# Kernel tuning notes

Hardware: AMD Instinct MI355X
Metric: run time of the kernel (lower is better)

The kernel has to match this reference:

```python
import jax, jax.numpy as jnp
import numpy as np
from jax import lax

BETA = 0.9   # membrane decay
THR = 1.0    # firing threshold (soft reset)
K = 10       # number of time bins
# spatial pyramid for original_shape=(100,368) under 4 stride-2 SAME convs
HW = [(50, 184), (25, 92), (13, 46), (7, 23)]
CH = [4, 8, 16, 32]


def conv(x, w, b, stride=1):
    y = lax.conv_general_dilated(x, w, (stride, stride), 'SAME',
                                 dimension_numbers=('NCHW', 'OIHW', 'NCHW'))
    return y + b[None, :, None, None]


def spike(u):
    # heaviside forward, sigmoid straight-through surrogate backward
    s = (u > 0.0).astype(u.dtype)
    sg = jax.nn.sigmoid(4.0 * u)
    return sg + lax.stop_gradient(s - sg)


def setup_inputs() -> dict:
    key = jax.random.key(0)
    ks = jax.random.split(key, 12)
    T, B = 1000, 1
    x = jax.random.normal(ks[0], (T, B, 1, 100, 368), jnp.float32)

    def w(k, o, i, kh=3, kw=3):
        return 0.1 * jax.random.normal(k, (o, i, kh, kw), jnp.float32)

    inp = {'x': x}
    cin = [1] + CH[:3]
    for li in range(4):
        inp['w%d' % (li + 1)] = w(ks[1 + li], CH[li], cin[li])
        inp['b%d' % (li + 1)] = jnp.zeros((CH[li],), jnp.float32)
    sc = [2 * K * c for c in CH]  # skip channels: [80,160,320,640]
    inp['dw4'] = w(ks[5], 64, sc[3]); inp['db4'] = jnp.zeros((64,), jnp.float32)
    inp['dw3'] = w(ks[6], 32, 64 + sc[2]); inp['db3'] = jnp.zeros((32,), jnp.float32)
    inp['dw2'] = w(ks[7], 16, 32 + sc[1]); inp['db2'] = jnp.zeros((16,), jnp.float32)
    inp['dw1'] = w(ks[8], 8, 16 + sc[0]); inp['db1'] = jnp.zeros((8,), jnp.float32)
    inp['wo'] = w(ks[9], 1, 8, 1, 1); inp['bo'] = jnp.zeros((1,), jnp.float32)
    inp['total_steps'] = 1000
    inp['block_size'] = 100
    return inp


def reference(x, w1, b1, w2, b2, w3, b3, w4, b4,
              dw4, db4, dw3, db3, dw2, db2, dw1, db1, wo, bo,
              total_steps, block_size):
    S = total_steps // K  # steps per bin
    B = x.shape[1]
    xb = x.reshape((K, S) + x.shape[1:])  # [K,S,B,C,H,W]
    mems0 = tuple(jnp.zeros((B, CH[i], HW[i][0], HW[i][1]), x.dtype) for i in range(4))
    enc_w = [(w1, b1), (w2, b2), (w3, b3), (w4, b4)]

    def forward_step(x_t, mems):
        new_mems, spk = [], x_t
        for (wi, bi), m in zip(enc_w, mems):
            m = BETA * m + conv(spk, wi, bi, 2)
            spk = spike(m - THR)
            m = m - spk * THR  # soft reset
            new_mems.append(m)
        return tuple(new_mems)

    def step(carry, x_t):
        mems, sums, sqs = carry
        mems = forward_step(x_t, mems)
        sums = tuple(s + m for s, m in zip(sums, mems))
        sqs = tuple(q + m * m for q, m in zip(sqs, mems))
        return (mems, sums, sqs), None

    def bin_fn(mems, x_bin):
        zeros = tuple(jnp.zeros_like(m) for m in mems)
        (mems, sums, sqs), _ = lax.scan(step, (mems, zeros, zeros), x_bin)
        means = tuple(s / S for s in sums)
        stds = tuple(jnp.sqrt(jnp.maximum(q / S - mu * mu, 1e-8))
                     for q, mu in zip(sqs, means))
        return mems, (means, stds)

    _, (means, stds) = lax.scan(bin_fn, mems0, xb)  # each leaf: [K,B,C,H,W]

    def skip(mean, std):
        # torch.cat([mean0,std0,mean1,std1,...], dim=1) channel ordering
        f = jnp.stack([mean, std], axis=1)        # [K,2,B,C,H,W]
        f = jnp.transpose(f, (2, 0, 1, 3, 4, 5))  # [B,K,2,C,H,W]
        b_, k_, t_, c_, h_, w_ = f.shape
        return f.reshape(b_, k_ * t_ * c_, h_, w_)

    skips = [skip(means[i], stds[i]) for i in range(4)]

    def up(t, hw):
        return jax.image.resize(t, (t.shape[0], t.shape[1], hw[0], hw[1]), 'bilinear')

    relu = jax.nn.relu
    d = relu(conv(skips[3], dw4, db4))
    d = relu(conv(jnp.concatenate([up(d, HW[2]), skips[2]], 1), dw3, db3))
    d = relu(conv(jnp.concatenate([up(d, HW[1]), skips[1]], 1), dw2, db2))
    d = relu(conv(jnp.concatenate([up(d, HW[0]), skips[0]], 1), dw1, db1))
    tau_c = conv(up(d, (100, 368)), wo, bo)  # [B,1,100,368]
    return tau_c
```

## Files before the change

### kernel.cpp

```cpp
#include <hip/hip_runtime.h>

#define KBINS  10
#define SBIN   100
#define BETA   0.9f
#define THR    1.0f
#define CDIV(a,b) (((a)+(b)-1)/(b))


__global__ void k_zero16(float4* __restrict__ p, int n16) {
    int i = blockIdx.x * blockDim.x + threadIdx.x;
    if (i < n16) p[i] = make_float4(0.f, 0.f, 0.f, 0.f);
}

__global__ void k_conv1(const float* __restrict__ x,
                        const float* __restrict__ w1,
                        const float* __restrict__ b1,
                        float* __restrict__ c1) {
    int n = blockIdx.x * blockDim.x + threadIdx.x;
    if (n >= 1000 * 50 * 46) return;
    int wq  = n % 46;
    int tmp = n / 46;
    int h   = tmp % 50;
    int t   = tmp / 50;
    int w0  = wq * 4;

    const float* xt = x + (size_t)t * 36800;
    float rm2 = (h  < 49)  ? 1.f : 0.f;
    float cm8 = (w0 < 180) ? 1.f : 0.f;
    int   r2  = min(2 * h + 2, 99);
    int   cb  = 2 * w0;
    int   c8  = min(cb + 8, 367);

    const float* row0 = xt + (2 * h) * 368 + cb;
    const float* row1 = row0 + 368;
    const float* row2 = xt + r2 * 368 + cb;

    float tap[3][9];
    #pragma unroll
    for (int j = 0; j < 8; j++) {
        tap[0][j] = row0[j];
        tap[1][j] = row1[j];
        tap[2][j] = row2[j] * rm2;
    }
    tap[0][8] = xt[(2 * h) * 368 + c8] * cm8;
    tap[1][8] = xt[(2 * h + 1) * 368 + c8] * cm8;
    tap[2][8] = xt[r2 * 368 + c8] * (rm2 * cm8);

    float* ot = c1 + (size_t)t * 36800 + h * 184 + w0;
    #pragma unroll
    for (int co = 0; co < 4; co++) {
        float b = b1[co];
        float a0 = b, a1 = b, a2 = b, a3 = b;
        #pragma unroll
        for (int r = 0; r < 3; r++) {
            #pragma unroll
            for (int kw = 0; kw < 3; kw++) {
                float wv = w1[co * 9 + r * 3 + kw];
                a0 = fmaf(tap[r][0 + kw], wv, a0);
                a1 = fmaf(tap[r][2 + kw], wv, a1);
                a2 = fmaf(tap[r][4 + kw], wv, a2);
                a3 = fmaf(tap[r][6 + kw], wv, a3);
            }
        }
        *(float4*)(ot + (size_t)co * 9200) = make_float4(a0, a1, a2, a3);
    }
}

__global__ void k_scan(const float* __restrict__ cbuf,
                       unsigned char* __restrict__ spk,
                       float* __restrict__ skip,
                       int C, int HW, int Win, int Wp, int HpWp, int write_spk) {
    const int PF = 10;
    int CHW = C * HW;
    int p = blockIdx.x * blockDim.x + threadIdx.x;
    if (p >= CHW) return;
    int c  = p / HW;
    int hw = p - c * HW;
    int h  = hw / Win, w = hw - h * Win;

    unsigned char* sp = spk + (size_t)c * HpWp + (h + 1) * Wp + (w + 1);
    const size_t tstr = (size_t)C * HpWp;

    float m = 0.0f;
    float va[PF], vb[PF];
    #pragma unroll
    for (int j = 0; j < PF; j++) va[j] = cbuf[(size_t)j * CHW + p];

    for (int k = 0; k < KBINS; k++) {
        float s = 0.0f, q = 0.0f;
        for (int b = 0; b < SBIN / PF; b++) {
            int t0 = k * SBIN + b * PF;
            int tn = t0 + PF;
            bool more = (tn < KBINS * SBIN);
            #pragma unroll
            for (int j = 0; j < PF; j++)
                vb[j] = more ? cbuf[(size_t)(tn + j) * CHW + p] : 0.0f;
            #pragma unroll
            for (int j = 0; j < PF; j++) {
                m = fmaf(m, BETA, va[j]);
                float spv = (m - THR > 0.0f) ? 1.0f : 0.0f;
                m -= spv * THR;
                if (write_spk) sp[(size_t)(t0 + j) * tstr] = (unsigned char)spv;
                s += m;
                q = fmaf(m, m, q);
            }
            #pragma unroll
            for (int j = 0; j < PF; j++) va[j] = vb[j];
        }
        float mean = s * (1.0f / SBIN);
        float var  = q * (1.0f / SBIN) - mean * mean;
        float sd   = sqrtf(fmaxf(var, 1e-8f));
        skip[(size_t)(k * 2 * C + c) * HW + hw]     = mean;
        skip[(size_t)(k * 2 * C + C + c) * HW + hw] = sd;
    }
}

template<int CIN, int COUT, int COG, int OW,
         int HOUT, int WOUT, int PADH, int HP, int WP>
__global__ void k_convs2(const unsigned char* __restrict__ spk,
                         const float* __restrict__ wt,
                         const float* __restrict__ bias,
                         float* __restrict__ out) {
    const int WQ = (WOUT + OW - 1) / OW;
    const int NT = 2 * OW + 1;
    int n = blockIdx.x * blockDim.x + threadIdx.x;
    if (n >= 1000 * HOUT * WQ) return;
    int wq  = n % WQ;
    int tmp = n / WQ;
    int h   = tmp % HOUT;
    int t   = tmp / HOUT;
    int cog = blockIdx.y;
    int w0  = wq * OW;

    const unsigned char* base = spk + (size_t)t * CIN * HP * WP
                              + (2 * h - PADH + 1) * WP + (2 * w0 + 1);

    float acc[OW][COG];
    #pragma unroll
    for (int q = 0; q < OW; q++)
        #pragma unroll
        for (int co = 0; co < COG; co++) acc[q][co] = bias[cog * COG + co];

    for (int ci = 0; ci < CIN; ci++) {
        const unsigned char* ic = base + (size_t)ci * HP * WP;
        float tap[3][NT];
        #pragma unroll
        for (int r = 0; r < 3; r++)
            #pragma unroll
            for (int j = 0; j < NT; j++)
                tap[r][j] = (float)ic[r * WP + j];
        #pragma unroll
        for (int co = 0; co < COG; co++) {
            const float* wc = wt + ((size_t)(cog * COG + co) * CIN + ci) * 9;
            #pragma unroll
            for (int r = 0; r < 3; r++)
                #pragma unroll
                for (int kw = 0; kw < 3; kw++) {
                    float wv = wc[r * 3 + kw];
                    #pragma unroll
                    for (int q = 0; q < OW; q++)
                        acc[q][co] = fmaf(tap[r][2 * q + kw], wv, acc[q][co]);
                }
        }
    }

    float* ot = out + ((size_t)t * COUT + cog * COG) * (HOUT * WOUT) + h * WOUT + w0;
    #pragma unroll
    for (int co = 0; co < COG; co++) {
        float* oc = ot + (size_t)co * (HOUT * WOUT);
        if constexpr (OW == 4) {
            *(float4*)oc = make_float4(acc[0][co], acc[1][co], acc[2][co], acc[3][co]);
        } else {
            if (w0 + 2 <= WOUT) *(float2*)oc = make_float2(acc[0][co], acc[1][co]);
            else                oc[0] = acc[0][co];
        }
    }
}

__global__ void k_conv_part(const float* __restrict__ in, int Cin, int H, int W,
                            const float* __restrict__ wt,
                            float* __restrict__ part,
                            int Cout, int CS) {
    int HW  = H * W;
    int pix = blockIdx.x * blockDim.x + threadIdx.x;
    if (pix >= HW) return;
    int co    = blockIdx.y;
    int chunk = blockIdx.z;
    int h = pix / W, w = pix - h * W;

    int off[9]; float msk[9];
    #pragma unroll
    for (int kh = 0; kh < 3; kh++) {
        int r = h + kh - 1;
        bool rok = (r >= 0) && (r < H);
        int rc = rok ? r : 0;
        #pragma unroll
        for (int kw = 0; kw < 3; kw++) {
            int cc = w + kw - 1;
            bool cok = (cc >= 0) && (cc < W);
            int ccc = cok ? cc : 0;
            off[kh * 3 + kw] = rc * W + ccc;
            msk[kh * 3 + kw] = (rok && cok) ? 1.0f : 0.0f;
        }
    }

    const float* ibase = in + (size_t)chunk * CS * HW;
    const float* wbase = wt + ((size_t)co * Cin + (size_t)chunk * CS) * 9;
    float acc = 0.0f;
    #pragma unroll 2
    for (int ci = 0; ci < CS; ci++) {
        const float* ic = ibase + (size_t)ci * HW;
        const float* wc = wbase + ci * 9;
        #pragma unroll
        for (int j = 0; j < 9; j++)
            acc = fmaf(msk[j] * ic[off[j]], wc[j], acc);
    }
    part[((size_t)chunk * Cout + co) * HW + pix] = acc;
}

__global__ void k_reduce_relu(const float* __restrict__ part,
                              const float* __restrict__ bias,
                              float* __restrict__ out,
                              int Cout, int HW, int nchunks) {
    int n = blockIdx.x * blockDim.x + threadIdx.x;
    if (n >= Cout * HW) return;
    int co = n / HW;
    float acc = bias[co];
    for (int c = 0; c < nchunks; c++)
        acc += part[(size_t)c * Cout * HW + n];
    out[n] = fmaxf(acc, 0.0f);
}

__global__ void k_up_cat(const float* __restrict__ up_src, int Cup, int Hi, int Wi,
                         const float* __restrict__ skip, int Cskip,
                         float* __restrict__ out, int Ho, int Wo) {
    int total = (Cup + Cskip) * Ho * Wo;
    int n = blockIdx.x * blockDim.x + threadIdx.x;
    if (n >= total) return;
    int w   = n % Wo;
    int tmp = n / Wo;
    int h   = tmp % Ho;
    int c   = tmp / Ho;
    float v;
    if (c < Cup) {
        float ph = (h + 0.5f) * (float)Hi / (float)Ho - 0.5f;
        float pw = (w + 0.5f) * (float)Wi / (float)Wo - 0.5f;
        float fh = floorf(ph), fw = floorf(pw);
        int h0 = (int)fh, w0 = (int)fw;
        float ah = ph - fh, aw = pw - fw;
        int h0c = min(max(h0, 0), Hi - 1), h1c = min(max(h0 + 1, 0), Hi - 1);
        int w0c = min(max(w0, 0), Wi - 1), w1c = min(max(w0 + 1, 0), Wi - 1);
        const float* sc = up_src + (size_t)c * Hi * Wi;
        float v00 = sc[h0c * Wi + w0c], v01 = sc[h0c * Wi + w1c];
        float v10 = sc[h1c * Wi + w0c], v11 = sc[h1c * Wi + w1c];
        v = (1.0f - ah) * ((1.0f - aw) * v00 + aw * v01)
          + ah * ((1.0f - aw) * v10 + aw * v11);
    } else {
        v = skip[(size_t)(c - Cup) * Ho * Wo + h * Wo + w];
    }
    out[n] = v;
}

__global__ void k_final(const float* __restrict__ d1,
                        const float* __restrict__ wo,
                        const float* __restrict__ bo,
                        float* __restrict__ out) {
    int n = blockIdx.x * blockDim.x + threadIdx.x;
    if (n >= 36800) return;
    int w = n % 368, h = n / 368;
    float ph = (h + 0.5f) * 0.5f - 0.5f;
    float pw = (w + 0.5f) * 0.5f - 0.5f;
    float fh = floorf(ph), fw = floorf(pw);
    int h0 = (int)fh, w0 = (int)fw;
    float ah = ph - fh, aw = pw - fw;
    int h0c = min(max(h0, 0), 49),  h1c = min(max(h0 + 1, 0), 49);
    int w0c = min(max(w0, 0), 183), w1c = min(max(w0 + 1, 0), 183);
    float acc = bo[0];
    #pragma unroll
    for (int c = 0; c < 8; c++) {
        const float* sc = d1 + c * 9200;
        float v00 = sc[h0c * 184 + w0c], v01 = sc[h0c * 184 + w1c];
        float v10 = sc[h1c * 184 + w0c], v11 = sc[h1c * 184 + w1c];
        float v = (1.0f - ah) * ((1.0f - aw) * v00 + aw * v01)
                + ah * ((1.0f - aw) * v10 + aw * v11);
        acc = fmaf(wo[c], v, acc);
    }
    out[n] = acc;
}

extern "C" void kernel_launch(void* const* d_in, const int* in_sizes, int n_in,
                              void* d_out, int out_size, void* d_ws, size_t ws_size,
                              hipStream_t stream) {
    (void)in_sizes; (void)n_in; (void)out_size; (void)ws_size;
    const float* x   = (const float*)d_in[0];
    const float* w1  = (const float*)d_in[1];
    const float* b1  = (const float*)d_in[2];
    const float* w2  = (const float*)d_in[3];
    const float* b2  = (const float*)d_in[4];
    const float* w3  = (const float*)d_in[5];
    const float* b3  = (const float*)d_in[6];
    const float* w4  = (const float*)d_in[7];
    const float* b4  = (const float*)d_in[8];
    const float* dw4 = (const float*)d_in[9];
    const float* db4 = (const float*)d_in[10];
    const float* dw3 = (const float*)d_in[11];
    const float* db3 = (const float*)d_in[12];
    const float* dw2 = (const float*)d_in[13];
    const float* db2 = (const float*)d_in[14];
    const float* dw1 = (const float*)d_in[15];
    const float* db1 = (const float*)d_in[16];
    const float* wo  = (const float*)d_in[17];
    const float* bo  = (const float*)d_in[18];
    float* out = (float*)d_out;

    char* ws = (char*)d_ws;
    size_t off = 0;
    auto alloc = [&](size_t bytes) -> void* {
        void* p = ws + off;
        off += (bytes + 255) & ~(size_t)255;
        return p;
    };
    float*         cbuf  = (float*)alloc(147200000);
    unsigned char* spk1p = (unsigned char*)alloc(39936000);
    unsigned char* spk2p = (unsigned char*)alloc(21600000);
    unsigned char* spk3p = (unsigned char*)alloc(12960000);
    float*         skip0 = (float*)alloc(2944000);
    float*         skip1 = (float*)alloc(1472000);
    float*         skip2 = (float*)alloc(765440);
    float*         skip3 = (float*)alloc(412160);
    char* dec = (char*)cbuf;
    size_t doff = 0;
    auto dalloc = [&](size_t bytes) -> void* {
        void* p = dec + doff;
        doff += (bytes + 255) & ~(size_t)255;
        return p;
    };
    float* d4   = (float*)dalloc(10304u * 4);
    float* cat3 = (float*)dalloc(229632u * 4);
    float* d3   = (float*)dalloc(19136u * 4);
    float* cat2 = (float*)dalloc(441600u * 4);
    float* d2   = (float*)dalloc(36800u * 4);
    float* cat1 = (float*)dalloc(883200u * 4);
    float* d1   = (float*)dalloc(73600u * 4);
    float* part = (float*)dalloc(1048576u);

    const int BS  = 256;
    const int SBS = 64;

    {
        int n16 = (39936000 + 21600000 + 12960000) / 16;
        k_zero16<<<CDIV(n16, BS), BS, 0, stream>>>((float4*)spk1p, n16);
    }

    k_conv1<<<CDIV(1000 * 50 * 46, BS), BS, 0, stream>>>(x, w1, b1, cbuf);
    k_scan<<<CDIV(36800, SBS), SBS, 0, stream>>>(cbuf, spk1p, skip0,
                                                 4, 9200, 184, 192, 52 * 192, 1);

    k_convs2<4, 8, 8, 4, 25, 92, 0, 52, 192>
        <<<dim3(CDIV(1000 * 25 * 23, BS), 1), BS, 0, stream>>>(spk1p, w2, b2, cbuf);
    k_scan<<<CDIV(18400, SBS), SBS, 0, stream>>>(cbuf, spk2p, skip1,
                                                 8, 2300, 92, 100, 27 * 100, 1);

    k_convs2<8, 16, 16, 2, 13, 46, 1, 27, 100>
        <<<dim3(CDIV(1000 * 13 * 23, BS), 1), BS, 0, stream>>>(spk2p, w3, b3, cbuf);
    k_scan<<<CDIV(9568, SBS), SBS, 0, stream>>>(cbuf, spk3p, skip2,
                                                16, 598, 46, 54, 15 * 54, 1);

    k_convs2<16, 32, 16, 2, 7, 23, 1, 15, 54>
        <<<dim3(CDIV(1000 * 7 * 12, BS), 2), BS, 0, stream>>>(spk3p, w4, b4, cbuf);
    k_scan<<<CDIV(5152, SBS), SBS, 0, stream>>>(cbuf, spk3p , skip3,
                                                32, 161, 23, 31, 9 * 31, 0);

    {
        dim3 g(CDIV(161, BS), 64, 10);
        k_conv_part<<<g, BS, 0, stream>>>(skip3, 640, 7, 23, dw4, part, 64, 64);
        k_reduce_relu<<<CDIV(64 * 161, BS), BS, 0, stream>>>(part, db4, d4, 64, 161, 10);
    }
    k_up_cat<<<CDIV(384 * 598, BS), BS, 0, stream>>>(d4, 64, 7, 23,
                                                     skip2, 320, cat3, 13, 46);
    {
        dim3 g(CDIV(598, BS), 32, 8);
        k_conv_part<<<g, BS, 0, stream>>>(cat3, 384, 13, 46, dw3, part, 32, 48);
        k_reduce_relu<<<CDIV(32 * 598, BS), BS, 0, stream>>>(part, db3, d3, 32, 598, 8);
    }
    k_up_cat<<<CDIV(192 * 2300, BS), BS, 0, stream>>>(d3, 32, 13, 46,
                                                      skip1, 160, cat2, 25, 92);
    {
        dim3 g(CDIV(2300, BS), 16, 4);
        k_conv_part<<<g, BS, 0, stream>>>(cat2, 192, 25, 92, dw2, part, 16, 48);
        k_reduce_relu<<<CDIV(16 * 2300, BS), BS, 0, stream>>>(part, db2, d2, 16, 2300, 4);
    }
    k_up_cat<<<CDIV(96 * 9200, BS), BS, 0, stream>>>(d2, 16, 25, 92,
                                                     skip0, 80, cat1, 50, 184);
    {
        dim3 g(CDIV(9200, BS), 8, 2);
        k_conv_part<<<g, BS, 0, stream>>>(cat1, 96, 50, 184, dw1, part, 8, 48);
        k_reduce_relu<<<CDIV(8 * 9200, BS), BS, 0, stream>>>(part, db1, d1, 8, 9200, 2);
    }
    k_final<<<CDIV(36800, BS), BS, 0, stream>>>(d1, wo, bo, out);
}
```

Measured before the change: 1.001 ms.

## Chunk encoder over time to shrink the conv buffer and fuse upsample-concat into decoder conv

The layer-1 and layer-2 conv plus scan stages now run in time chunks (5 and 2 chunks), with membrane state carried between chunks, so the fp32 conv buffer shrinks from about 147 MB to about 38 MB and can stay more cache-resident. The separate upsample/concat kernels are removed; a new decoder conv kernel computes the bilinear upsample on the fly and reads skip features directly. The cost is more kernel launches, serial dependencies between chunks, and repeated interpolation work inside the conv. Some decoder block sizes also change and the partial-conv loop uses two accumulators.

```diff
diff --git a/kernel.cpp b/kernel.cpp
--- a/kernel.cpp
+++ b/kernel.cpp
@@ -15,9 +15,9 @@
 __global__ void k_conv1(const float* __restrict__ x,
                         const float* __restrict__ w1,
                         const float* __restrict__ b1,
-                        float* __restrict__ c1) {
+                        float* __restrict__ c1, int tcount) {
     int n = blockIdx.x * blockDim.x + threadIdx.x;
-    if (n >= 1000 * 50 * 46) return;
+    if (n >= tcount * 50 * 46) return;
     int wq  = n % 46;
     int tmp = n / 46;
     int h   = tmp % 50;
@@ -69,7 +69,9 @@
 __global__ void k_scan(const float* __restrict__ cbuf,
                        unsigned char* __restrict__ spk,
                        float* __restrict__ skip,
-                       int C, int HW, int Win, int Wp, int HpWp, int write_spk) {
+                       float* __restrict__ mstate,
+                       int C, int HW, int Win, int Wp, int HpWp,
+                       int write_spk, int bin0, int nbins, int init) {
     const int PF = 10;
     int CHW = C * HW;
     int p = blockIdx.x * blockDim.x + threadIdx.x;
@@ -78,41 +80,45 @@
     int hw = p - c * HW;
     int h  = hw / Win, w = hw - h * Win;
 
-    unsigned char* sp = spk + (size_t)c * HpWp + (h + 1) * Wp + (w + 1);
     const size_t tstr = (size_t)C * HpWp;
-
-    float m = 0.0f;
+    unsigned char* sp = spk + (size_t)bin0 * SBIN * tstr
+                      + (size_t)c * HpWp + (h + 1) * Wp + (w + 1);
+
+    float m = init ? 0.0f : mstate[p];
     float va[PF], vb[PF];
     #pragma unroll
     for (int j = 0; j < PF; j++) va[j] = cbuf[(size_t)j * CHW + p];
 
-    for (int k = 0; k < KBINS; k++) {
+    int T = nbins * SBIN;
+    for (int k = 0; k < nbins; k++) {
         float s = 0.0f, q = 0.0f;
         for (int b = 0; b < SBIN / PF; b++) {
-            int t0 = k * SBIN + b * PF;
-            int tn = t0 + PF;
-            bool more = (tn < KBINS * SBIN);
+            int lt0 = k * SBIN + b * PF;
+            int ltn = lt0 + PF;
+            bool more = (ltn < T);
             #pragma unroll
             for (int j = 0; j < PF; j++)
-                vb[j] = more ? cbuf[(size_t)(tn + j) * CHW + p] : 0.0f;
+                vb[j] = more ? cbuf[(size_t)(ltn + j) * CHW + p] : 0.0f;
             #pragma unroll
             for (int j = 0; j < PF; j++) {
                 m = fmaf(m, BETA, va[j]);
                 float spv = (m - THR > 0.0f) ? 1.0f : 0.0f;
                 m -= spv * THR;
-                if (write_spk) sp[(size_t)(t0 + j) * tstr] = (unsigned char)spv;
+                if (write_spk) sp[(size_t)(lt0 + j) * tstr] = (unsigned char)spv;
                 s += m;
                 q = fmaf(m, m, q);
             }
             #pragma unroll
             for (int j = 0; j < PF; j++) va[j] = vb[j];
         }
+        int g = bin0 + k;
         float mean = s * (1.0f / SBIN);
         float var  = q * (1.0f / SBIN) - mean * mean;
         float sd   = sqrtf(fmaxf(var, 1e-8f));
-        skip[(size_t)(k * 2 * C + c) * HW + hw]     = mean;
-        skip[(size_t)(k * 2 * C + C + c) * HW + hw] = sd;
-    }
+        skip[(size_t)(g * 2 * C + c) * HW + hw]     = mean;
+        skip[(size_t)(g * 2 * C + C + c) * HW + hw] = sd;
+    }
+    mstate[p] = m;
 }
 
 template<int CIN, int COUT, int COG, int OW,
@@ -120,19 +126,19 @@
 __global__ void k_convs2(const unsigned char* __restrict__ spk,
                          const float* __restrict__ wt,
                          const float* __restrict__ bias,
-                         float* __restrict__ out) {
+                         float* __restrict__ out, int t0, int tcount) {
     const int WQ = (WOUT + OW - 1) / OW;
     const int NT = 2 * OW + 1;
     int n = blockIdx.x * blockDim.x + threadIdx.x;
-    if (n >= 1000 * HOUT * WQ) return;
+    if (n >= tcount * HOUT * WQ) return;
     int wq  = n % WQ;
     int tmp = n / WQ;
     int h   = tmp % HOUT;
-    int t   = tmp / HOUT;
+    int tl  = tmp / HOUT;
     int cog = blockIdx.y;
     int w0  = wq * OW;
 
-    const unsigned char* base = spk + (size_t)t * CIN * HP * WP
+    const unsigned char* base = spk + (size_t)(t0 + tl) * CIN * HP * WP
                               + (2 * h - PADH + 1) * WP + (2 * w0 + 1);
 
     float acc[OW][COG];
@@ -164,7 +170,7 @@
         }
     }
 
-    float* ot = out + ((size_t)t * COUT + cog * COG) * (HOUT * WOUT) + h * WOUT + w0;
+    float* ot = out + ((size_t)tl * COUT + cog * COG) * (HOUT * WOUT) + h * WOUT + w0;
     #pragma unroll
     for (int co = 0; co < COG; co++) {
         float* oc = ot + (size_t)co * (HOUT * WOUT);
@@ -206,16 +212,99 @@
 
     const float* ibase = in + (size_t)chunk * CS * HW;
     const float* wbase = wt + ((size_t)co * Cin + (size_t)chunk * CS) * 9;
-    float acc = 0.0f;
-    #pragma unroll 2
-    for (int ci = 0; ci < CS; ci++) {
-        const float* ic = ibase + (size_t)ci * HW;
-        const float* wc = wbase + ci * 9;
+    float acc0 = 0.0f, acc1 = 0.0f;
+    for (int ci = 0; ci < CS; ci += 2) {
+        const float* ic0 = ibase + (size_t)ci * HW;
+        const float* wc0 = wbase + ci * 9;
         #pragma unroll
         for (int j = 0; j < 9; j++)
-            acc = fmaf(msk[j] * ic[off[j]], wc[j], acc);
-    }
-    part[((size_t)chunk * Cout + co) * HW + pix] = acc;
+            acc0 = fmaf(msk[j] * ic0[off[j]], wc0[j], acc0);
+        const float* ic1 = ic0 + HW;
+        const float* wc1 = wc0 + 9;
+        #pragma unroll
+        for (int j = 0; j < 9; j++)
+            acc1 = fmaf(msk[j] * ic1[off[j]], wc1[j], acc1);
+    }
+    part[((size_t)chunk * Cout + co) * HW + pix] = acc0 + acc1;
+}
+
+__global__ void k_dconv_part(const float* __restrict__ skp, int Cskip,
+                             const float* __restrict__ dprev, int Cup,
+                             int Hi, int Wi,
+                             const float* __restrict__ wt,
+                             float* __restrict__ part,
+                             int Cout, int CS, int H, int W) {
+    int HW  = H * W;
+    int pix = blockIdx.x * blockDim.x + threadIdx.x;
+    if (pix >= HW) return;
+    int co    = blockIdx.y;
+    int chunk = blockIdx.z;
+    int h = pix / W, w = pix - h * W;
+    int Cin = Cup + Cskip;
+
+    int roff[3], h0c[3], h1c[3];
+    float rmsk[3], ah[3];
+    #pragma unroll
+    for (int kh = 0; kh < 3; kh++) {
+        int r = h + kh - 1;
+        bool rok = (r >= 0) && (r < H);
+        roff[kh] = rok ? r : 0;
+        rmsk[kh] = rok ? 1.0f : 0.0f;
+        float ph = (r + 0.5f) * (float)Hi / (float)H - 0.5f;
+        float fh = floorf(ph);
+        ah[kh] = ph - fh;
+        int hh = (int)fh;
+        h0c[kh] = min(max(hh, 0), Hi - 1);
+        h1c[kh] = min(max(hh + 1, 0), Hi - 1);
+    }
+    int coff[3], w0c[3], w1c[3];
+    float cmsk[3], aw[3];
+    #pragma unroll
+    for (int kw = 0; kw < 3; kw++) {
+        int cc = w + kw - 1;
+        bool cok = (cc >= 0) && (cc < W);
+        coff[kw] = cok ? cc : 0;
+        cmsk[kw] = cok ? 1.0f : 0.0f;
+        float pw = (cc + 0.5f) * (float)Wi / (float)W - 0.5f;
+        float fw = floorf(pw);
+        aw[kw] = pw - fw;
+        int ww = (int)fw;
+        w0c[kw] = min(max(ww, 0), Wi - 1);
+        w1c[kw] = min(max(ww + 1, 0), Wi - 1);
+    }
+
+    float acc0 = 0.0f, acc1 = 0.0f;
+    for (int cl = 0; cl < CS; cl++) {
+        int ci = chunk * CS + cl;
+        const float* wc = wt + ((size_t)co * Cin + ci) * 9;
+        float a = 0.0f;
+        if (ci < Cup) {
+            const float* dc = dprev + (size_t)ci * Hi * Wi;
+            #pragma unroll
+            for (int kh = 0; kh < 3; kh++) {
+                #pragma unroll
+                for (int kw = 0; kw < 3; kw++) {
+                    float v00 = dc[h0c[kh] * Wi + w0c[kw]];
+                    float v01 = dc[h0c[kh] * Wi + w1c[kw]];
+                    float v10 = dc[h1c[kh] * Wi + w0c[kw]];
+                    float v11 = dc[h1c[kh] * Wi + w1c[kw]];
+                    float v = (1.0f - ah[kh]) * ((1.0f - aw[kw]) * v00 + aw[kw] * v01)
+                            + ah[kh] * ((1.0f - aw[kw]) * v10 + aw[kw] * v11);
+                    a = fmaf(v * rmsk[kh] * cmsk[kw], wc[kh * 3 + kw], a);
+                }
+            }
+        } else {
+            const float* ic = skp + (size_t)(ci - Cup) * HW;
+            #pragma unroll
+            for (int kh = 0; kh < 3; kh++)
+                #pragma unroll
+                for (int kw = 0; kw < 3; kw++)
+                    a = fmaf(rmsk[kh] * cmsk[kw] * ic[roff[kh] * W + coff[kw]],
+                             wc[kh * 3 + kw], a);
+        }
+        if (cl & 1) acc1 += a; else acc0 += a;
+    }
+    part[((size_t)chunk * Cout + co) * HW + pix] = acc0 + acc1;
 }
 
 __global__ void k_reduce_relu(const float* __restrict__ part,
@@ -229,36 +318,6 @@
     for (int c = 0; c < nchunks; c++)
         acc += part[(size_t)c * Cout * HW + n];
     out[n] = fmaxf(acc, 0.0f);
-}
-
-__global__ void k_up_cat(const float* __restrict__ up_src, int Cup, int Hi, int Wi,
-                         const float* __restrict__ skip, int Cskip,
-                         float* __restrict__ out, int Ho, int Wo) {
-    int total = (Cup + Cskip) * Ho * Wo;
-    int n = blockIdx.x * blockDim.x + threadIdx.x;
-    if (n >= total) return;
-    int w   = n % Wo;
-    int tmp = n / Wo;
-    int h   = tmp % Ho;
-    int c   = tmp / Ho;
-    float v;
-    if (c < Cup) {
-        float ph = (h + 0.5f) * (float)Hi / (float)Ho - 0.5f;
-        float pw = (w + 0.5f) * (float)Wi / (float)Wo - 0.5f;
-        float fh = floorf(ph), fw = floorf(pw);
-        int h0 = (int)fh, w0 = (int)fw;
-        float ah = ph - fh, aw = pw - fw;
-        int h0c = min(max(h0, 0), Hi - 1), h1c = min(max(h0 + 1, 0), Hi - 1);
-        int w0c = min(max(w0, 0), Wi - 1), w1c = min(max(w0 + 1, 0), Wi - 1);
-        const float* sc = up_src + (size_t)c * Hi * Wi;
-        float v00 = sc[h0c * Wi + w0c], v01 = sc[h0c * Wi + w1c];
-        float v10 = sc[h1c * Wi + w0c], v11 = sc[h1c * Wi + w1c];
-        v = (1.0f - ah) * ((1.0f - aw) * v00 + aw * v01)
-          + ah * ((1.0f - aw) * v10 + aw * v11);
-    } else {
-        v = skip[(size_t)(c - Cup) * Ho * Wo + h * Wo + w];
-    }
-    out[n] = v;
 }
 
 __global__ void k_final(const float* __restrict__ d1,
@@ -320,7 +379,7 @@
         off += (bytes + 255) & ~(size_t)255;
         return p;
     };
-    float*         cbuf  = (float*)alloc(147200000);
+    float*         cbuf  = (float*)alloc(38272000);
     unsigned char* spk1p = (unsigned char*)alloc(39936000);
     unsigned char* spk2p = (unsigned char*)alloc(21600000);
     unsigned char* spk3p = (unsigned char*)alloc(12960000);
@@ -328,6 +387,8 @@
     float*         skip1 = (float*)alloc(1472000);
     float*         skip2 = (float*)alloc(765440);
     float*         skip3 = (float*)alloc(412160);
+    float*         ms1   = (float*)alloc(147200);
+    float*         ms2   = (float*)alloc(73600);
     char* dec = (char*)cbuf;
     size_t doff = 0;
     auto dalloc = [&](size_t bytes) -> void* {
@@ -336,13 +397,10 @@
         return p;
     };
     float* d4   = (float*)dalloc(10304u * 4);
-    float* cat3 = (float*)dalloc(229632u * 4);
     float* d3   = (float*)dalloc(19136u * 4);
-    float* cat2 = (float*)dalloc(441600u * 4);
     float* d2   = (float*)dalloc(36800u * 4);
-    float* cat1 = (float*)dalloc(883200u * 4);
     float* d1   = (float*)dalloc(73600u * 4);
-    float* part = (float*)dalloc(1048576u);
+    float* part = (float*)dalloc(2500000u);
 
     const int BS  = 256;
     const int SBS = 64;
@@ -352,49 +410,57 @@
         k_zero16<<<CDIV(n16, BS), BS, 0, stream>>>((float4*)spk1p, n16);
     }
 
-    k_conv1<<<CDIV(1000 * 50 * 46, BS), BS, 0, stream>>>(x, w1, b1, cbuf);
-    k_scan<<<CDIV(36800, SBS), SBS, 0, stream>>>(cbuf, spk1p, skip0,
-                                                 4, 9200, 184, 192, 52 * 192, 1);
-
-    k_convs2<4, 8, 8, 4, 25, 92, 0, 52, 192>
-        <<<dim3(CDIV(1000 * 25 * 23, BS), 1), BS, 0, stream>>>(spk1p, w2, b2, cbuf);
-    k_scan<<<CDIV(18400, SBS), SBS, 0, stream>>>(cbuf, spk2p, skip1,
-                                                 8, 2300, 92, 100, 27 * 100, 1);
+    for (int q = 0; q < 5; q++) {
+        k_conv1<<<CDIV(200 * 50 * 46, BS), BS, 0, stream>>>(
+            x + (size_t)q * 200 * 36800, w1, b1, cbuf, 200);
+        k_scan<<<CDIV(36800, SBS), SBS, 0, stream>>>(
+            cbuf, spk1p, skip0, ms1, 4, 9200, 184, 192, 52 * 192,
+            1, 2 * q, 2, (q == 0) ? 1 : 0);
+    }
+
+    for (int q = 0; q < 2; q++) {
+        k_convs2<4, 8, 8, 4, 25, 92, 0, 52, 192>
+            <<<dim3(CDIV(500 * 25 * 23, BS), 1), BS, 0, stream>>>(
+                spk1p, w2, b2, cbuf, q * 500, 500);
+        k_scan<<<CDIV(18400, SBS), SBS, 0, stream>>>(
+            cbuf, spk2p, skip1, ms2, 8, 2300, 92, 100, 27 * 100,
+            1, 5 * q, 5, (q == 0) ? 1 : 0);
+    }
 
     k_convs2<8, 16, 16, 2, 13, 46, 1, 27, 100>
-        <<<dim3(CDIV(1000 * 13 * 23, BS), 1), BS, 0, stream>>>(spk2p, w3, b3, cbuf);
-    k_scan<<<CDIV(9568, SBS), SBS, 0, stream>>>(cbuf, spk3p, skip2,
-                                                16, 598, 46, 54, 15 * 54, 1);
+        <<<dim3(CDIV(1000 * 13 * 23, BS), 1), BS, 0, stream>>>(
+            spk2p, w3, b3, cbuf, 0, 1000);
+    k_scan<<<CDIV(9568, SBS), SBS, 0, stream>>>(
+        cbuf, spk3p, skip2, ms2, 16, 598, 46, 54, 15 * 54, 1, 0, 10, 1);
 
     k_convs2<16, 32, 16, 2, 7, 23, 1, 15, 54>
-        <<<dim3(CDIV(1000 * 7 * 12, BS), 2), BS, 0, stream>>>(spk3p, w4, b4, cbuf);
-    k_scan<<<CDIV(5152, SBS), SBS, 0, stream>>>(cbuf, spk3p , skip3,
-                                                32, 161, 23, 31, 9 * 31, 0);
+        <<<dim3(CDIV(1000 * 7 * 12, BS), 2), BS, 0, stream>>>(
+            spk3p, w4, b4, cbuf, 0, 1000);
+    k_scan<<<CDIV(5152, SBS), SBS, 0, stream>>>(
+        cbuf, spk3p , skip3, ms1 , 32, 161, 23, 31, 9 * 31,
+        0, 0, 10, 1);
 
     {
-        dim3 g(CDIV(161, BS), 64, 10);
-        k_conv_part<<<g, BS, 0, stream>>>(skip3, 640, 7, 23, dw4, part, 64, 64);
+        dim3 g(CDIV(161, 64), 64, 10);
+        k_conv_part<<<g, 64, 0, stream>>>(skip3, 640, 7, 23, dw4, part, 64, 64);
         k_reduce_relu<<<CDIV(64 * 161, BS), BS, 0, stream>>>(part, db4, d4, 64, 161, 10);
     }
-    k_up_cat<<<CDIV(384 * 598, BS), BS, 0, stream>>>(d4, 64, 7, 23,
-                                                     skip2, 320, cat3, 13, 46);
     {
-        dim3 g(CDIV(598, BS), 32, 8);
-        k_conv_part<<<g, BS, 0, stream>>>(cat3, 384, 13, 46, dw3, part, 32, 48);
+        dim3 g(CDIV(598, 64), 32, 8);
+        k_dconv_part<<<g, 64, 0, stream>>>(skip2, 320, d4, 64, 7, 23,
+                                           dw3, part, 32, 48, 13, 46);
         k_reduce_relu<<<CDIV(32 * 598, BS), BS, 0, stream>>>(part, db3, d3, 32, 598, 8);
     }
-    k_up_cat<<<CDIV(192 * 2300, BS), BS, 0, stream>>>(d3, 32, 13, 46,
-                                                      skip1, 160, cat2, 25, 92);
     {
         dim3 g(CDIV(2300, BS), 16, 4);
-        k_conv_part<<<g, BS, 0, stream>>>(cat2, 192, 25, 92, dw2, part, 16, 48);
+        k_dconv_part<<<g, BS, 0, stream>>>(skip1, 160, d3, 32, 13, 46,
+                                           dw2, part, 16, 48, 25, 92);
         k_reduce_relu<<<CDIV(16 * 2300, BS), BS, 0, stream>>>(part, db2, d2, 16, 2300, 4);
     }
-    k_up_cat<<<CDIV(96 * 9200, BS), BS, 0, stream>>>(d2, 16, 25, 92,
-                                                     skip0, 80, cat1, 50, 184);
     {
         dim3 g(CDIV(9200, BS), 8, 2);
-        k_conv_part<<<g, BS, 0, stream>>>(cat1, 96, 50, 184, dw1, part, 8, 48);
+        k_dconv_part<<<g, BS, 0, stream>>>(skip0, 80, d2, 16, 25, 92,
+                                           dw1, part, 8, 48, 50, 184);
         k_reduce_relu<<<CDIV(8 * 9200, BS), BS, 0, stream>>>(part, db1, d1, 8, 9200, 2);
     }
     k_final<<<CDIV(36800, BS), BS, 0, stream>>>(d1, wo, bo, out);
```

After: 968.2 us. 1.03x faster.
